# Performance work log

Hardware: AMD Instinct MI355X
Metric: run time of the kernel (lower is better)

## Reference

```python
import jax, jax.numpy as jnp
import numpy as np

NUM_NODES = 262144        # 1024 graphs x 256 nodes
NODES_PER_GRAPH = 256
NUM_GRAPHS = NUM_NODES // NODES_PER_GRAPH
NUM_EDGES = 2097152       # avg degree 8
NUM_FEATURES = 9
NUM_STATIONS = 8


def setup_inputs() -> dict:
    key = jax.random.key(0)
    ks = jax.random.split(key, 12)
    # edges constrained within each graph so batched-graph semantics hold
    src_local = jax.random.randint(ks[0], (NUM_EDGES,), 0, NODES_PER_GRAPH)
    dst_local = jax.random.randint(ks[1], (NUM_EDGES,), 0, NODES_PER_GRAPH)
    graph_of_edge = jax.random.randint(ks[2], (NUM_EDGES,), 0, NUM_GRAPHS)
    offset = graph_of_edge * NODES_PER_GRAPH
    edge_index = jnp.stack([src_local + offset, dst_local + offset]).astype(jnp.int64)
    station_ids = jnp.array([0, 37, 73, 110, 146, 183, 219, 255], dtype=jnp.int64)
    s = lambda k, shape, fan_in: jax.random.normal(k, shape, jnp.float32) / np.sqrt(fan_in)
    return {
        "x": jax.random.normal(ks[3], (NUM_NODES, NUM_FEATURES), jnp.float32),
        "edge_index": edge_index,
        "station_ids": station_ids,
        "W1": s(ks[4], (NUM_FEATURES, 32), NUM_FEATURES),
        "b1": jnp.zeros((32,), jnp.float32),
        "W2": s(ks[5], (32, 64), 32),
        "b2": jnp.zeros((64,), jnp.float32),
        "fc1_W": s(ks[6], (128, 64), 128),
        "fc1_b": jnp.zeros((64,), jnp.float32),
        "fc2_W": s(ks[7], (64, 1), 64),
        "fc2_b": jnp.zeros((1,), jnp.float32),
    }


def _gcn_conv(x, W, b, src, dst, n_nodes):
    """PyG GCNConv: add self-loops, symmetric normalization, linear first."""
    h = x @ W                                              # [N, C_out]
    # degree includes the self-loop (+1), counted on target nodes
    deg = jnp.zeros((n_nodes,), h.dtype).at[dst].add(1.0) + 1.0
    dinv = jax.lax.rsqrt(deg)                              # deg >= 1, safe
    norm = dinv[src] * dinv[dst]                           # [E]
    out = jnp.zeros_like(h).at[dst].add(norm[:, None] * h[src])
    out = out + (dinv * dinv)[:, None] * h                 # self-loop term
    return out + b


def reference(x, edge_index, station_ids, W1, b1, W2, b2, fc1_W, fc1_b, fc2_W, fc2_b):
    n = x.shape[0]
    src, dst = edge_index[0], edge_index[1]
    h = jax.nn.relu(_gcn_conv(x, W1, b1, src, dst, n))     # [N, 32]
    h = jax.nn.relu(_gcn_conv(h, W2, b2, src, dst, n))     # [N, 64]
    # global mean pool per graph (batch = node_idx // NODES_PER_GRAPH)
    batch = jnp.arange(n) // NODES_PER_GRAPH
    sums = jax.ops.segment_sum(h, batch, num_segments=NUM_GRAPHS)
    counts = jax.ops.segment_sum(jnp.ones((n,), h.dtype), batch, num_segments=NUM_GRAPHS)
    global_ctx = sums / counts[:, None]                    # [B, 64]
    # per-station gather-MLP, vectorized over stations
    idx = jnp.arange(NUM_GRAPHS)[:, None] * NODES_PER_GRAPH + station_ids[None, :]  # [B, S]
    station_emb = h[idx]                                   # [B, S, 64]
    ctx = jnp.broadcast_to(global_ctx[:, None, :], station_emb.shape)
    combined = jnp.concatenate([station_emb, ctx], axis=-1)  # [B, S, 128]
    q = jax.nn.relu(combined @ fc1_W + fc1_b) @ fc2_W + fc2_b  # [B, S, 1]
    return q[..., 0]                                       # [B, S]
```

## Files before the change

kernel.cpp:

```cpp
#include <hip/hip_runtime.h>
#include <hip/hip_bf16.h>


#define NNODES 262144
#define NPG 256
#define NGRAPHS 1024
#define NEDGES 2097152
#define NFEAT 9
#define ECAP2 2560
#define T_EDGES 8192
#define NTILES (NEDGES / T_EDGES)
#define TPB 1024
#define NBLK 256
#define EBSTRIDE 4608

typedef __hip_bfloat16 bf16;
typedef short short8 __attribute__((ext_vector_type(8)));
typedef float f32x4 __attribute__((ext_vector_type(4)));

__device__ __forceinline__ float bfbits(unsigned short u) { return __uint_as_float(((unsigned)u) << 16); }
__device__ __forceinline__ unsigned short f2bbits(float v) { bf16 b = __float2bfloat16(v); return *(unsigned short*)&b; }


__global__ void __launch_bounds__(1024) k_hist(const int* __restrict__ dst,
                                               int* __restrict__ hist) {
    __shared__ int cnt[NGRAPHS];
    int t = threadIdx.x;
    cnt[t] = 0;
    __syncthreads();
    const int4* d4 = (const int4*)(dst + blockIdx.x * T_EDGES);
#pragma unroll
    for (int k = 0; k < T_EDGES / 4096; ++k) {
        int4 dv = d4[k * 1024 + t];
        atomicAdd(&cnt[dv.x >> 8], 1);
        atomicAdd(&cnt[dv.y >> 8], 1);
        atomicAdd(&cnt[dv.z >> 8], 1);
        atomicAdd(&cnt[dv.w >> 8], 1);
    }
    __syncthreads();
    hist[blockIdx.x * NGRAPHS + t] = cnt[t];
}

__global__ void __launch_bounds__(256) k_scan(int* __restrict__ hist,
                                              int* __restrict__ gcnt) {
    __shared__ int wsum[4];
    int g = blockIdx.x;
    int t = threadIdx.x;
    int lane = t & 63, wv = t >> 6;
    int v = hist[t * NGRAPHS + g];
    int inc = v;
    for (int off = 1; off < 64; off <<= 1) {
        int y = __shfl_up(inc, off);
        if (lane >= off) inc += y;
    }
    if (lane == 63) wsum[wv] = inc;
    __syncthreads();
    int wpre = 0;
#pragma unroll
    for (int w = 0; w < 3; ++w) if (w < wv) wpre += wsum[w];
    int exc = wpre + inc - v;
    hist[t * NGRAPHS + g] = exc;
    if (t == 255) gcnt[g * 16] = exc + v;
}

__global__ void __launch_bounds__(1024) k_scatter(const int* __restrict__ src,
                                                  const int* __restrict__ dst,
                                                  const int* __restrict__ hist,
                                                  unsigned short* __restrict__ gout) {
    __shared__ unsigned short sg[T_EDGES];
    __shared__ unsigned short pay[T_EDGES];
    __shared__ unsigned short spay[T_EDGES];
    __shared__ unsigned short ssg[T_EDGES];
    __shared__ int cnt[NGRAPHS];
    __shared__ int lbase[NGRAPHS];
    __shared__ int gb[NGRAPHS];
    __shared__ int wsum[16];
    int t = threadIdx.x;
    int lane = t & 63, wv = t >> 6;
    int base = blockIdx.x * T_EDGES;
    cnt[t] = 0;
    gb[t] = hist[blockIdx.x * NGRAPHS + t];
    __syncthreads();
    const int4* s4 = (const int4*)(src + base);
    const int4* d4 = (const int4*)(dst + base);
#pragma unroll
    for (int k = 0; k < T_EDGES / 4096; ++k) {
        int idx = k * 1024 + t;
        int4 dv = d4[idx];
        int4 sv = s4[idx];
        int i0 = idx * 4;
        sg[i0]     = (unsigned short)(dv.x >> 8);
        sg[i0 + 1] = (unsigned short)(dv.y >> 8);
        sg[i0 + 2] = (unsigned short)(dv.z >> 8);
        sg[i0 + 3] = (unsigned short)(dv.w >> 8);
        pay[i0]     = (unsigned short)(((dv.x & 255) << 8) | (sv.x & 255));
        pay[i0 + 1] = (unsigned short)(((dv.y & 255) << 8) | (sv.y & 255));
        pay[i0 + 2] = (unsigned short)(((dv.z & 255) << 8) | (sv.z & 255));
        pay[i0 + 3] = (unsigned short)(((dv.w & 255) << 8) | (sv.w & 255));
        atomicAdd(&cnt[dv.x >> 8], 1);
        atomicAdd(&cnt[dv.y >> 8], 1);
        atomicAdd(&cnt[dv.z >> 8], 1);
        atomicAdd(&cnt[dv.w >> 8], 1);
    }
    __syncthreads();
    int c = cnt[t];
    int inc = c;
    for (int off = 1; off < 64; off <<= 1) {
        int y = __shfl_up(inc, off);
        if (lane >= off) inc += y;
    }
    if (lane == 63) wsum[wv] = inc;
    __syncthreads();
    int wpre = 0;
    for (int w = 0; w < wv; ++w) wpre += wsum[w];
    lbase[t] = wpre + inc - c;
    cnt[t] = 0;
    __syncthreads();
#pragma unroll
    for (int k = 0; k < T_EDGES / 1024; ++k) {
        int i = k * 1024 + t;
        int g = sg[i];
        int p = lbase[g] + atomicAdd(&cnt[g], 1);
        spay[p] = pay[i];
        ssg[p] = (unsigned short)g;
    }
    __syncthreads();
#pragma unroll
    for (int k = 0; k < T_EDGES / 1024; ++k) {
        int p = k * 1024 + t;
        int g = ssg[p];
        int off = gb[g] + (p - lbase[g]);
        if (off < ECAP2) gout[(size_t)g * ECAP2 + off] = spay[p];
    }
}

__global__ void __launch_bounds__(256) k_sort2(const int* __restrict__ gcnt,
                                               const unsigned short* __restrict__ gout,
                                               unsigned char* __restrict__ eblob) {
    __shared__ unsigned short ep[ECAP2];
    __shared__ unsigned int cnt[256];
    __shared__ unsigned int base[256];
    __shared__ int wsum[4];
    int g = blockIdx.x;
    int t = threadIdx.x;
    int lane = t & 63, wv = t >> 6;
    int ecnt = min(gcnt[g * 16], ECAP2);
    cnt[t] = 0;
    {
        const uint4* gev = (const uint4*)(gout + (size_t)g * ECAP2);
        uint4* epv = (uint4*)ep;
        for (int i = t; i < ECAP2 / 8; i += 256) epv[i] = gev[i];
    }
    __syncthreads();
    for (int i = t; i < ecnt; i += 256) atomicAdd(&cnt[ep[i] >> 8], 1u);
    __syncthreads();
    int c = (int)cnt[t];
    int inc = c;
    for (int off = 1; off < 64; off <<= 1) {
        int y = __shfl_up(inc, off);
        if (lane >= off) inc += y;
    }
    if (lane == 63) wsum[wv] = inc;
    __syncthreads();
    int wpre = 0;
    for (int w = 0; w < wv; ++w) wpre += wsum[w];
    int exc = wpre + inc - c;
    unsigned char* eb = eblob + (size_t)g * EBSTRIDE;
    ((unsigned short*)(eb + 3584))[t] = (unsigned short)exc;
    if (t == 255) ((unsigned short*)(eb + 3584))[256] = (unsigned short)(exc + c);
    ((float*)(eb + 2560))[t] = rsqrtf((float)(c + 1));
    base[t] = (unsigned)exc;
    __syncthreads();
    for (int i = t; i < ecnt; i += 256) {
        unsigned short v = ep[i];
        unsigned p = atomicAdd(&base[v >> 8], 1u);
        if (p < ECAP2) eb[p] = (unsigned char)(v & 255);
    }
}


__global__ void __launch_bounds__(TPB) k_fused(
    const float* __restrict__ x, const int* __restrict__ station_ids,
    const float* __restrict__ W1, const float* __restrict__ b1,
    const float* __restrict__ W2, const float* __restrict__ b2,
    const float* __restrict__ fc1W, const float* __restrict__ fc1b,
    const float* __restrict__ fc2W, const float* __restrict__ fc2b,
    const unsigned char* __restrict__ eblob, float* __restrict__ out) {

    __shared__ __align__(16) unsigned char Ms[131072];
    __shared__ __align__(16) unsigned char Buf[16384];
    __shared__ __align__(16) unsigned char El[ECAP2];
    __shared__ __align__(16) float dinvs[256];
    __shared__ __align__(4) unsigned short Rl[260];
    __shared__ float W1s[288];
    __shared__ float sts[512];
    __shared__ float poolf[64];
    __shared__ float spart[8];
    __shared__ unsigned char stmap[256];
    __shared__ float b1s[32], b2s[64], fc1bs[64], fc2ws[64];
    __shared__ int stids[8];
    __shared__ float fc2bv;

    int t = threadIdx.x;
    int lane = t & 63, wvid = t >> 6;
    int m = lane & 15, quad = lane >> 4;

    for (int i = t; i < NFEAT * 32; i += TPB) W1s[i] = W1[i];
    if (t < 32) b1s[t] = b1[t];
    if (t < 64) { b2s[t] = b2[t]; fc1bs[t] = fc1b[t]; fc2ws[t] = fc2W[t]; poolf[t] = 0.f; }
    if (t < 8) { stids[t] = station_ids[t]; spart[t] = 0.f; }
    if (t == 0) fc2bv = fc2b[0];
    if (t < 256) stmap[t] = 255;
    short8 w2f[4];
#pragma unroll
    for (int ni = 0; ni < 4; ++ni)
#pragma unroll
        for (int j = 0; j < 8; ++j)
            w2f[ni][j] = (short)f2bbits(W2[(quad * 8 + j) * 64 + ni * 16 + m]);
    short8 fc1f[4];
    {
        int ni = wvid & 3;
#pragma unroll
        for (int kt = 0; kt < 4; ++kt)
#pragma unroll
            for (int j = 0; j < 8; ++j)
                fc1f[kt][j] = (short)f2bbits(fc1W[((kt * 4 + quad) * 8 + j) * 64 + ni * 16 + m]);
    }
    __syncthreads();
    if (t < 8) stmap[stids[t] & 255] = (unsigned char)t;

    for (int g = blockIdx.x; g < NGRAPHS; g += NBLK) {

        {
            const unsigned char* eb = eblob + (size_t)g * EBSTRIDE;
            const uint4* ev = (const uint4*)eb;
            const uint4* dv = (const uint4*)(eb + 2560);
            const unsigned int* rv = (const unsigned int*)(eb + 3584);
            for (int i = t; i < 160; i += TPB) ((uint4*)El)[i] = ev[i];
            for (int i = t; i < 64; i += TPB) ((uint4*)dinvs)[i] = dv[i];
            for (int i = t; i < 129; i += TPB) ((unsigned int*)Rl)[i] = rv[i];
        }
        __syncthreads();

        if (t < 512) {
            int d = t >> 1, q = t & 1;
            uint4* mz = (uint4*)(Ms + d * 512 + q * 256);
            uint4 z = {0u, 0u, 0u, 0u};
#pragma unroll
            for (int i = 0; i < 16; ++i) mz[i] = z;
            float did = dinvs[d];
            if ((d >> 7) == q)
                *(unsigned short*)(Ms + d * 512 + (((d >> 3) ^ (d & 15)) * 16) + (d & 7) * 2)
                    = f2bbits(did * did);
            int r0 = Rl[d], r1 = Rl[d + 1];
            for (int e = r0; e < r1; ++e) {
                int s = El[e];
                if ((s >> 7) == q) {
                    unsigned short* p =
                        (unsigned short*)(Ms + d * 512 + (((s >> 3) ^ (d & 15)) * 16) + (s & 7) * 2);
                    *p = f2bbits(bfbits(*p) + did * dinvs[s]);
                }
            }
        } else {
            int tt = t - 512;
            int n = tt >> 1, half = tt & 1;
            const float* xr = x + (size_t)(g * NPG + n) * NFEAT;
            float xv[NFEAT];
#pragma unroll
            for (int k = 0; k < NFEAT; ++k) xv[k] = xr[k];
            int c0 = half * 16;
#pragma unroll 4
            for (int ci = 0; ci < 16; ++ci) {
                int c = c0 + ci;
                float acc = 0.f;
#pragma unroll
                for (int k = 0; k < NFEAT; ++k) acc += xv[k] * W1s[k * 32 + c];
                *(unsigned short*)(Buf + c * 512 + (((n >> 3) ^ (c & 15)) * 16) + (n & 7) * 2)
                    = f2bbits(acc);
            }
        }
        __syncthreads();

        f32x4 acc1[2] = {};
        for (int kt = 0; kt < 8; ++kt) {
            short8 af = *(const short8*)(Ms + (size_t)(wvid * 16 + m) * 512 + (((kt * 4 + quad) ^ m) * 16));
            short8 bf0 = *(const short8*)(Buf + (size_t)m * 512 + (((kt * 4 + quad) ^ m) * 16));
            short8 bf1 = *(const short8*)(Buf + (size_t)(16 + m) * 512 + (((kt * 4 + quad) ^ m) * 16));
            acc1[0] = __builtin_amdgcn_mfma_f32_16x16x32_bf16(af, bf0, acc1[0], 0, 0, 0);
            acc1[1] = __builtin_amdgcn_mfma_f32_16x16x32_bf16(af, bf1, acc1[1], 0, 0, 0);
        }
        __syncthreads();

#pragma unroll
        for (int ct = 0; ct < 2; ++ct) {
            int ch = ct * 16 + m;
            float bb = b1s[ch];
#pragma unroll
            for (int r = 0; r < 4; ++r) {
                int node = wvid * 16 + quad * 4 + r;
                *(unsigned short*)(Buf + (size_t)ch * 512 + (((node >> 3) ^ (ch & 15)) * 16) + (node & 7) * 2)
                    = f2bbits(fmaxf(acc1[ct][r] + bb, 0.f));
            }
        }
        __syncthreads();

        {
            f32x4 a2[2] = {};
            for (int kt = 0; kt < 8; ++kt) {
                short8 af = *(const short8*)(Ms + (size_t)(wvid * 16 + m) * 512 + (((kt * 4 + quad) ^ m) * 16));
                short8 bf0 = *(const short8*)(Buf + (size_t)m * 512 + (((kt * 4 + quad) ^ m) * 16));
                short8 bf1 = *(const short8*)(Buf + (size_t)(16 + m) * 512 + (((kt * 4 + quad) ^ m) * 16));
                a2[0] = __builtin_amdgcn_mfma_f32_16x16x32_bf16(af, bf0, a2[0], 0, 0, 0);
                a2[1] = __builtin_amdgcn_mfma_f32_16x16x32_bf16(af, bf1, a2[1], 0, 0, 0);
            }
#pragma unroll
            for (int ct = 0; ct < 2; ++ct) {
                int ch = ct * 16 + m;
                int c8 = ch >> 3;
#pragma unroll
                for (int r = 0; r < 4; ++r) {
                    int node = wvid * 16 + quad * 4 + r;
                    *(unsigned short*)(Ms + (size_t)node * 512 + ((c8 ^ (node & 3)) * 16) + (ch & 7) * 2)
                        = f2bbits(a2[ct][r]);
                }
            }
        }
        __syncthreads();

        {
            int mt = wvid;
            short8 af = *(const short8*)(Ms + (size_t)(mt * 16 + m) * 512 + ((quad ^ (m & 3)) * 16));
#pragma unroll
            for (int ni = 0; ni < 4; ++ni) {
                f32x4 c = {};
                c = __builtin_amdgcn_mfma_f32_16x16x32_bf16(af, w2f[ni], c, 0, 0, 0);
                int ch = ni * 16 + m;
                float bb = b2s[ch];
                float hv[4];
                float p = 0.f;
#pragma unroll
                for (int r = 0; r < 4; ++r) { hv[r] = fmaxf(c[r] + bb, 0.f); p += hv[r]; }
                p += __shfl_down(p, 32);
                p += __shfl_down(p, 16);
                if (quad == 0) atomicAdd(&poolf[ch], p);
#pragma unroll
                for (int r = 0; r < 4; ++r) {
                    int node = mt * 16 + quad * 4 + r;
                    int si = stmap[node];
                    if (si != 255) sts[si * 64 + ch] = hv[r];
                }
            }
        }
        __syncthreads();

        if (wvid < 4) {
            short8 af4[4];
#pragma unroll
            for (int kt = 0; kt < 4; ++kt) {
#pragma unroll
                for (int j = 0; j < 8; ++j) {
                    int k = kt * 32 + quad * 8 + j;
                    float v = 0.f;
                    if (m < 8) v = (k < 64) ? sts[m * 64 + k] : poolf[k - 64] * (1.0f / 256.0f);
                    af4[kt][j] = (short)f2bbits(v);
                }
            }
            f32x4 c = {};
#pragma unroll
            for (int kt = 0; kt < 4; ++kt)
                c = __builtin_amdgcn_mfma_f32_16x16x32_bf16(af4[kt], fc1f[kt], c, 0, 0, 0);
            int ch = wvid * 16 + m;
            float fb = fc1bs[ch], fw = fc2ws[ch];
#pragma unroll
            for (int r = 0; r < 4; ++r) {
                float a = fmaxf(c[r] + fb, 0.f) * fw;
#pragma unroll
                for (int off = 1; off < 16; off <<= 1) a += __shfl_xor(a, off);
                int st = quad * 4 + r;
                if (m == 0 && st < 8) atomicAdd(&spart[st], a);
            }
        }
        __syncthreads();

        if (t < 8) { out[g * 8 + t] = spart[t] + fc2bv; spart[t] = 0.f; }
        if (t >= 64 && t < 128) poolf[t - 64] = 0.f;
    }
}


extern "C" void kernel_launch(void* const* d_in, const int* in_sizes, int n_in,
                              void* d_out, int out_size, void* d_ws, size_t ws_size,
                              hipStream_t stream) {
    const float* x = (const float*)d_in[0];
    const int* ei = (const int*)d_in[1];
    const int* station_ids = (const int*)d_in[2];
    const float* W1 = (const float*)d_in[3];
    const float* b1 = (const float*)d_in[4];
    const float* W2 = (const float*)d_in[5];
    const float* bias2 = (const float*)d_in[6];
    const float* fc1W = (const float*)d_in[7];
    const float* fc1b = (const float*)d_in[8];
    const float* fc2W = (const float*)d_in[9];
    const float* fc2b = (const float*)d_in[10];
    float* out = (float*)d_out;
    (void)in_sizes; (void)n_in; (void)out_size; (void)ws_size;

    char* ws = (char*)d_ws;
    int* gcnt = (int*)ws;
    unsigned short* gout = (unsigned short*)(ws + 0x10000);
    int* hist = (int*)(ws + 0x510000);
    unsigned char* eblob = (unsigned char*)(ws + 0x610000);

    const int* esrc = ei;
    const int* edst = ei + NEDGES;

    k_hist<<<NTILES, 1024, 0, stream>>>(edst, hist);
    k_scan<<<NGRAPHS, 256, 0, stream>>>(hist, gcnt);
    k_scatter<<<NTILES, 1024, 0, stream>>>(esrc, edst, hist, gout);
    k_sort2<<<NGRAPHS, 256, 0, stream>>>(gcnt, gout, eblob);
    k_fused<<<NBLK, TPB, 0, stream>>>(x, station_ids, W1, b1, W2, bias2,
                                      fc1W, fc1b, fc2W, fc2b, eblob, out);
}
```

Baseline: 167.7 us.

## Prefetch next graph's edge blob during MLP stage and rotate zero-fill stores

Moves the per-graph load of edge list, dinv and row pointers out of the loop head. The first graph is loaded before the loop, and each next graph is loaded by otherwise idle threads (t>=256) during the final MLP stage. This removes one barrier per graph and hides global load latency behind compute. It also staggers the zeroing of each LDS row by thread index, likely to reduce bank conflicts. The risk is that El, dinvs and Rl get overwritten while still in use, which is only safe if no earlier stage reads them after the preceding barrier.

After: 161.1 us, median of 2. 1.04x faster.

```diff
diff --git a/kernel.cpp b/kernel.cpp
--- a/kernel.cpp
+++ b/kernel.cpp
@@ -226,28 +226,26 @@
             for (int j = 0; j < 8; ++j)
                 fc1f[kt][j] = (short)f2bbits(fc1W[((kt * 4 + quad) * 8 + j) * 64 + ni * 16 + m]);
     }
+    {
+        const unsigned char* eb = eblob + (size_t)blockIdx.x * EBSTRIDE;
+        for (int i = t; i < 160; i += TPB) ((uint4*)El)[i] = ((const uint4*)eb)[i];
+        for (int i = t; i < 64; i += TPB) ((uint4*)dinvs)[i] = ((const uint4*)(eb + 2560))[i];
+        for (int i = t; i < 129; i += TPB) ((unsigned int*)Rl)[i] = ((const unsigned int*)(eb + 3584))[i];
+    }
     __syncthreads();
     if (t < 8) stmap[stids[t] & 255] = (unsigned char)t;
 
     for (int g = blockIdx.x; g < NGRAPHS; g += NBLK) {
-
-        {
-            const unsigned char* eb = eblob + (size_t)g * EBSTRIDE;
-            const uint4* ev = (const uint4*)eb;
-            const uint4* dv = (const uint4*)(eb + 2560);
-            const unsigned int* rv = (const unsigned int*)(eb + 3584);
-            for (int i = t; i < 160; i += TPB) ((uint4*)El)[i] = ev[i];
-            for (int i = t; i < 64; i += TPB) ((uint4*)dinvs)[i] = dv[i];
-            for (int i = t; i < 129; i += TPB) ((unsigned int*)Rl)[i] = rv[i];
-        }
-        __syncthreads();
 
         if (t < 512) {
             int d = t >> 1, q = t & 1;
-            uint4* mz = (uint4*)(Ms + d * 512 + q * 256);
+            unsigned char* rowp = Ms + d * 512 + q * 256;
             uint4 z = {0u, 0u, 0u, 0u};
 #pragma unroll
-            for (int i = 0; i < 16; ++i) mz[i] = z;
+            for (int i = 0; i < 16; ++i) {
+                int cc = (i + t) & 15;
+                *(uint4*)(rowp + cc * 16) = z;
+            }
             float did = dinvs[d];
             if ((d >> 7) == q)
                 *(unsigned short*)(Ms + d * 512 + (((d >> 3) ^ (d & 15)) * 16) + (d & 7) * 2)
@@ -329,11 +327,11 @@
 
         {
             int mt = wvid;
-            short8 af = *(const short8*)(Ms + (size_t)(mt * 16 + m) * 512 + ((quad ^ (m & 3)) * 16));
+            short8 af2 = *(const short8*)(Ms + (size_t)(mt * 16 + m) * 512 + ((quad ^ (m & 3)) * 16));
 #pragma unroll
             for (int ni = 0; ni < 4; ++ni) {
                 f32x4 c = {};
-                c = __builtin_amdgcn_mfma_f32_16x16x32_bf16(af, w2f[ni], c, 0, 0, 0);
+                c = __builtin_amdgcn_mfma_f32_16x16x32_bf16(af2, w2f[ni], c, 0, 0, 0);
                 int ch = ni * 16 + m;
                 float bb = b2s[ch];
                 float hv[4];
@@ -378,6 +376,15 @@
                 for (int off = 1; off < 16; off <<= 1) a += __shfl_xor(a, off);
                 int st = quad * 4 + r;
                 if (m == 0 && st < 8) atomicAdd(&spart[st], a);
+            }
+        } else {
+            int gn = g + NBLK;
+            if (gn < NGRAPHS) {
+                const unsigned char* eb = eblob + (size_t)gn * EBSTRIDE;
+                int ts = t - 256;
+                for (int i = ts; i < 160; i += 768) ((uint4*)El)[i] = ((const uint4*)eb)[i];
+                for (int i = ts; i < 64; i += 768) ((uint4*)dinvs)[i] = ((const uint4*)(eb + 2560))[i];
+                for (int i = ts; i < 129; i += 768) ((unsigned int*)Rl)[i] = ((const unsigned int*)(eb + 3584))[i];
             }
         }
         __syncthreads();
```
